# Kernel optimization log

Hardware: AMD Instinct MI355X
Metric: run time of the kernel (lower is better)

The kernel has to match this reference:

```python
import jax, jax.numpy as jnp
import numpy as np

K = 16  # number of piecewise-linear intervals (fixed in params_set)


def setup_inputs() -> dict:
    key = jax.random.key(0)
    k1, k2 = jax.random.split(key)
    B, S, D = 4, 4096, 2048
    x = jax.random.normal(k1, (B, S, D), dtype=jnp.float32)
    threshold = jnp.ones((1,), dtype=jnp.float32)          # alpha > 0
    theta = 0.1 * jax.random.normal(k2, (K,), dtype=jnp.float32)
    dst = jnp.arange(K, dtype=jnp.float32) / K             # delta * arange(K), delta = 1/K
    return {
        "x": x,
        "threshold": threshold,
        "theta": theta,
        "dst": dst,
        "Qn": 0,
        "Qp": 15,                 # 2**4 - 1 (activation, num_bits=4)
        "num_elements": B * S * D,
    }


def reference(x, threshold, theta, dst, Qn, Qp, num_elements):
    # LCQ_quantizer.forward (non 2-bit-weight path) -> LCQ_fast_core.forward
    s = float(Qp)
    theta_tmp = jax.nn.softmax(theta)                       # softmax over dim 0
    gamma = theta_tmp * K                                   # theta_tmp / delta
    beta = jnp.concatenate(
        [jnp.zeros((1,), theta_tmp.dtype), jnp.cumsum(theta_tmp)[: K - 1]]
    )
    alpha = threshold                                       # shape (1,), broadcasts

    flag_middle = (jnp.abs(x) < alpha).astype(x.dtype)
    flag_high = 1.0 - flag_middle
    x_tmp = jnp.abs(x) / alpha

    # compress: searchsorted bin lookup + piecewise affine
    idx = jnp.searchsorted(dst, x_tmp, side="right")        # in [1, K]
    y = gamma[idx - 1] * (x_tmp - dst[idx - 1]) + beta[idx - 1]
    y_q = jnp.round(y * s) / s                              # uniform round-quantize

    # expand: second searchsorted + inverse affine
    idx_q = jnp.searchsorted(beta, y_q, side="right")       # in [1, K]
    z_mid = (y_q - beta[idx_q - 1]) / gamma[idx_q - 1] + dst[idx_q - 1]

    z = jnp.sign(x) * alpha * (z_mid * flag_middle + flag_high)
    return z
```

## Files before the change

### kernel.cpp

```cpp
#include <hip/hip_runtime.h>
#include <math.h>

#define KB 16

typedef float vf4 __attribute__((ext_vector_type(4)));

__device__ __forceinline__ float lcq_core(float xv, float alpha, float rcp_alpha,
                                          const float2* s_gb,
                                          const float* s_pv)
{
    float a   = fabsf(xv);
    float xt  = __fmul_rn(a, rcp_alpha);
    float t16 = __fmul_rn(xt, 16.0f);
    float jf  = fminf(t16, 15.0f);
    int   j   = (int)jf;
    float2 gb = s_gb[j];
    float dj  = __fmul_rn(floorf(jf), 0.0625f);
    float y   = __fadd_rn(__fmul_rn(gb.x, __fsub_rn(xt, dj)), gb.y);
    float t   = rintf(__fmul_rn(y, 15.0f));
    int   m   = (int)fminf(t, 15.0f);
    float r   = (a < alpha) ? s_pv[m] : alpha;
    return copysignf(r, xv);
}

__global__ __launch_bounds__(256) void lcq_kernel(
    const float* __restrict__ x,
    const float* __restrict__ thr,
    const float* __restrict__ theta,
    float* __restrict__ out,
    long long n)
{
    __shared__ float s_tab[4][64];

    const long long n4ll = n >> 2;
    const vf4* __restrict__ x4 = (const vf4*)x;
    vf4* __restrict__ o4 = (vf4*)out;

    float th[KB];
    #pragma unroll
    for (int i = 0; i < KB; ++i) th[i] = theta[i];
    const float alpha = thr[0];
    const float rcpa  = __fdiv_rn(1.0f, alpha);

    const unsigned base = blockIdx.x * 2048u + threadIdx.x;
    const bool full = ((long long)(blockIdx.x + 1) * 2048ll <= n4ll);

    vf4 v0, v1, v2, v3, v4, v5, v6, v7;
    if (full) {
        v0 = __builtin_nontemporal_load(&x4[base]);
        v1 = __builtin_nontemporal_load(&x4[base +  256u]);
        v2 = __builtin_nontemporal_load(&x4[base +  512u]);
        v3 = __builtin_nontemporal_load(&x4[base +  768u]);
        v4 = __builtin_nontemporal_load(&x4[base + 1024u]);
        v5 = __builtin_nontemporal_load(&x4[base + 1280u]);
        v6 = __builtin_nontemporal_load(&x4[base + 1536u]);
        v7 = __builtin_nontemporal_load(&x4[base + 1792u]);
    }

    float* tab = s_tab[threadIdx.x >> 6];
    if ((threadIdx.x & 63) == 0) {
        float mx = th[0];
        #pragma unroll
        for (int i = 1; i < KB; ++i) mx = fmaxf(mx, th[i]);
        float ex[KB];
        float sum = 0.0f;
        #pragma unroll
        for (int i = 0; i < KB; ++i) { ex[i] = expf(__fsub_rn(th[i], mx)); sum = __fadd_rn(sum, ex[i]); }
        float sm[KB];
        #pragma unroll
        for (int i = 0; i < KB; ++i) sm[i] = __fdiv_rn(ex[i], sum);

        float beta[KB], gamma[KB];
        beta[0] = 0.0f;
        float c = sm[0];
        #pragma unroll
        for (int i = 1; i < KB; ++i) { beta[i] = c; c = __fadd_rn(c, sm[i]); }
        #pragma unroll
        for (int i = 0; i < KB; ++i) gamma[i] = __fmul_rn(sm[i], 16.0f);

        #pragma unroll
        for (int i = 0; i < KB; ++i) ((float2*)tab)[i] = make_float2(gamma[i], beta[i]);

        for (int m = 0; m < KB; ++m) {
            float yq = __fdiv_rn((float)m, 15.0f);
            int iq = 0;
            #pragma unroll
            for (int i = 1; i < KB; ++i) iq += (beta[i] <= yq) ? 1 : 0;
            float zv = __fadd_rn(__fdiv_rn(__fsub_rn(yq, beta[iq]), gamma[iq]),
                                 (float)iq * 0.0625f);
            tab[32 + m] = __fmul_rn(alpha, zv);
        }
    }
    const float2* gbp = (const float2*)tab;
    const float*  pvp = tab + 32;

    if (full) {
#define LCQ_CS(V, off) { \
        vf4 r; \
        r.x = lcq_core(V.x, alpha, rcpa, gbp, pvp); \
        r.y = lcq_core(V.y, alpha, rcpa, gbp, pvp); \
        r.z = lcq_core(V.z, alpha, rcpa, gbp, pvp); \
        r.w = lcq_core(V.w, alpha, rcpa, gbp, pvp); \
        __builtin_nontemporal_store(r, &o4[base + (off)]); }
        LCQ_CS(v0, 0u)
        LCQ_CS(v1, 256u)
        LCQ_CS(v2, 512u)
        LCQ_CS(v3, 768u)
        LCQ_CS(v4, 1024u)
        LCQ_CS(v5, 1280u)
        LCQ_CS(v6, 1536u)
        LCQ_CS(v7, 1792u)
#undef LCQ_CS
    } else {
        #pragma unroll
        for (int k = 0; k < 8; ++k) {
            long long i = (long long)base + k * 256;
            if (i < n4ll) {
                vf4 v = x4[i];
                vf4 r;
                r.x = lcq_core(v.x, alpha, rcpa, gbp, pvp);
                r.y = lcq_core(v.y, alpha, rcpa, gbp, pvp);
                r.z = lcq_core(v.z, alpha, rcpa, gbp, pvp);
                r.w = lcq_core(v.w, alpha, rcpa, gbp, pvp);
                o4[i] = r;
            }
        }
        if (blockIdx.x == gridDim.x - 1) {
            for (long long k = (n4ll << 2) + threadIdx.x; k < n; k += 256) {
                out[k] = lcq_core(x[k], alpha, rcpa, gbp, pvp);
            }
        }
    }
}

extern "C" void kernel_launch(void* const* d_in, const int* in_sizes, int n_in,
                              void* d_out, int out_size, void* d_ws, size_t ws_size,
                              hipStream_t stream) {
    const float* x     = (const float*)d_in[0];
    const float* thr   = (const float*)d_in[1];
    const float* theta = (const float*)d_in[2];
    float* out = (float*)d_out;

    long long n = (long long)in_sizes[0];
    long long n4 = n >> 2;
    long long grid = (n4 + 2047) / 2048;
    if (grid < 1) grid = 1;
    dim3 block(256);
    hipLaunchKernelGGL(lcq_kernel, dim3((unsigned)grid), block, 0, stream,
                       x, thr, theta, out, n);
}
```

Before: 233.9 us.

## Process two 2048-vector chunks per block and fold 1/16 scaling into table

Each block now handles 4096 float4 vectors in two sequential batches of eight loads, halving the grid. This spreads the per-block theta load, softmax and table build over twice as much data. The per-element math is also rescaled: alpha's reciprocal is pre-multiplied by 16 and gamma by 1/16, which drops one multiply per element. The trade-offs are that the second batch's loads are only issued after the first batch is processed, so less memory is in flight per block, and the rescaled arithmetic may differ slightly in rounding.

```diff
diff --git a/kernel.cpp b/kernel.cpp
--- a/kernel.cpp
+++ b/kernel.cpp
@@ -5,18 +5,17 @@
 
 typedef float vf4 __attribute__((ext_vector_type(4)));
 
-__device__ __forceinline__ float lcq_core(float xv, float alpha, float rcp_alpha,
+__device__ __forceinline__ float lcq_core(float xv, float alpha, float rcpa16,
                                           const float2* s_gb,
                                           const float* s_pv)
 {
     float a   = fabsf(xv);
-    float xt  = __fmul_rn(a, rcp_alpha);
-    float t16 = __fmul_rn(xt, 16.0f);
+    float t16 = __fmul_rn(a, rcpa16);
     float jf  = fminf(t16, 15.0f);
     int   j   = (int)jf;
     float2 gb = s_gb[j];
-    float dj  = __fmul_rn(floorf(jf), 0.0625f);
-    float y   = __fadd_rn(__fmul_rn(gb.x, __fsub_rn(xt, dj)), gb.y);
+    float fj  = floorf(jf);
+    float y   = __fadd_rn(__fmul_rn(gb.x, __fsub_rn(t16, fj)), gb.y);
     float t   = rintf(__fmul_rn(y, 15.0f));
     int   m   = (int)fminf(t, 15.0f);
     float r   = (a < alpha) ? s_pv[m] : alpha;
@@ -39,14 +38,15 @@
     float th[KB];
     #pragma unroll
     for (int i = 0; i < KB; ++i) th[i] = theta[i];
-    const float alpha = thr[0];
-    const float rcpa  = __fdiv_rn(1.0f, alpha);
+    const float alpha  = thr[0];
+    const float rcpa   = __fdiv_rn(1.0f, alpha);
+    const float rcpa16 = __fmul_rn(rcpa, 16.0f);
 
-    const unsigned base = blockIdx.x * 2048u + threadIdx.x;
-    const bool full = ((long long)(blockIdx.x + 1) * 2048ll <= n4ll);
+    const unsigned base = blockIdx.x * 4096u + threadIdx.x;
 
+    const bool full0 = ((long long)blockIdx.x * 4096ll + 2048ll <= n4ll);
     vf4 v0, v1, v2, v3, v4, v5, v6, v7;
-    if (full) {
+    if (full0) {
         v0 = __builtin_nontemporal_load(&x4[base]);
         v1 = __builtin_nontemporal_load(&x4[base +  256u]);
         v2 = __builtin_nontemporal_load(&x4[base +  512u]);
@@ -79,7 +79,8 @@
         for (int i = 0; i < KB; ++i) gamma[i] = __fmul_rn(sm[i], 16.0f);
 
         #pragma unroll
-        for (int i = 0; i < KB; ++i) ((float2*)tab)[i] = make_float2(gamma[i], beta[i]);
+        for (int i = 0; i < KB; ++i)
+            ((float2*)tab)[i] = make_float2(__fmul_rn(gamma[i], 0.0625f), beta[i]);
 
         for (int m = 0; m < KB; ++m) {
             float yq = __fdiv_rn((float)m, 15.0f);
@@ -94,14 +95,15 @@
     const float2* gbp = (const float2*)tab;
     const float*  pvp = tab + 32;
 
-    if (full) {
 #define LCQ_CS(V, off) { \
         vf4 r; \
-        r.x = lcq_core(V.x, alpha, rcpa, gbp, pvp); \
-        r.y = lcq_core(V.y, alpha, rcpa, gbp, pvp); \
-        r.z = lcq_core(V.z, alpha, rcpa, gbp, pvp); \
-        r.w = lcq_core(V.w, alpha, rcpa, gbp, pvp); \
+        r.x = lcq_core(V.x, alpha, rcpa16, gbp, pvp); \
+        r.y = lcq_core(V.y, alpha, rcpa16, gbp, pvp); \
+        r.z = lcq_core(V.z, alpha, rcpa16, gbp, pvp); \
+        r.w = lcq_core(V.w, alpha, rcpa16, gbp, pvp); \
         __builtin_nontemporal_store(r, &o4[base + (off)]); }
+
+    if (full0) {
         LCQ_CS(v0, 0u)
         LCQ_CS(v1, 256u)
         LCQ_CS(v2, 512u)
@@ -110,24 +112,47 @@
         LCQ_CS(v5, 1280u)
         LCQ_CS(v6, 1536u)
         LCQ_CS(v7, 1792u)
+    }
+
+    const bool full1 = ((long long)blockIdx.x * 4096ll + 4096ll <= n4ll);
+    if (full1) {
+        v0 = __builtin_nontemporal_load(&x4[base + 2048u]);
+        v1 = __builtin_nontemporal_load(&x4[base + 2304u]);
+        v2 = __builtin_nontemporal_load(&x4[base + 2560u]);
+        v3 = __builtin_nontemporal_load(&x4[base + 2816u]);
+        v4 = __builtin_nontemporal_load(&x4[base + 3072u]);
+        v5 = __builtin_nontemporal_load(&x4[base + 3328u]);
+        v6 = __builtin_nontemporal_load(&x4[base + 3584u]);
+        v7 = __builtin_nontemporal_load(&x4[base + 3840u]);
+        LCQ_CS(v0, 2048u)
+        LCQ_CS(v1, 2304u)
+        LCQ_CS(v2, 2560u)
+        LCQ_CS(v3, 2816u)
+        LCQ_CS(v4, 3072u)
+        LCQ_CS(v5, 3328u)
+        LCQ_CS(v6, 3584u)
+        LCQ_CS(v7, 3840u)
+    }
 #undef LCQ_CS
-    } else {
-        #pragma unroll
-        for (int k = 0; k < 8; ++k) {
-            long long i = (long long)base + k * 256;
+
+    if (!full0 || !full1) {
+        const int k0 = full0 ? 8 : 0;
+        #pragma unroll 1
+        for (int k = k0; k < 16; ++k) {
+            long long i = (long long)base + (long long)k * 256;
             if (i < n4ll) {
                 vf4 v = x4[i];
                 vf4 r;
-                r.x = lcq_core(v.x, alpha, rcpa, gbp, pvp);
-                r.y = lcq_core(v.y, alpha, rcpa, gbp, pvp);
-                r.z = lcq_core(v.z, alpha, rcpa, gbp, pvp);
-                r.w = lcq_core(v.w, alpha, rcpa, gbp, pvp);
+                r.x = lcq_core(v.x, alpha, rcpa16, gbp, pvp);
+                r.y = lcq_core(v.y, alpha, rcpa16, gbp, pvp);
+                r.z = lcq_core(v.z, alpha, rcpa16, gbp, pvp);
+                r.w = lcq_core(v.w, alpha, rcpa16, gbp, pvp);
                 o4[i] = r;
             }
         }
         if (blockIdx.x == gridDim.x - 1) {
             for (long long k = (n4ll << 2) + threadIdx.x; k < n; k += 256) {
-                out[k] = lcq_core(x[k], alpha, rcpa, gbp, pvp);
+                out[k] = lcq_core(x[k], alpha, rcpa16, gbp, pvp);
             }
         }
     }
@@ -143,7 +168,7 @@
 
     long long n = (long long)in_sizes[0];
     long long n4 = n >> 2;
-    long long grid = (n4 + 2047) / 2048;
+    long long grid = (n4 + 4095) / 4096;
     if (grid < 1) grid = 1;
     dim3 block(256);
     hipLaunchKernelGGL(lcq_kernel, dim3((unsigned)grid), block, 0, stream,
```

Measured after the change: 235.6 us. No clear change (+0.7%).
